# Performance work log

Measured on AMD Instinct MI355X. Metric: run time of the kernel, lower is better.

Reference implementation:

```python
import math
import jax, jax.numpy as jnp
import numpy as np

L = 3
EPS = 1e-06


def _geometry(H, W, L):
    """Replicates the Python-side region layout of the torch ramac() exactly."""
    ovr = 0.4
    steps = np.array([2, 3, 4, 5, 6, 7], dtype=np.float64)
    w = min(W, H)
    b = (max(H, W) - w) / (steps - 1)
    idx = int(np.argmin(np.abs((w ** 2 - w * b) / w ** 2 - ovr)))
    Wd = idx if H < W else 0
    Hd = idx if H > W else 0
    regions = []  # list of (i, j, wl) static ints
    for l in range(1, L + 1):
        wl = math.floor(2 * w / (l + 1))
        if wl == 0:
            continue
        wl2 = math.floor(wl / 2 - 1)
        bW = 0 if l + Wd == 1 else (W - wl) / (l + Wd - 1)
        cenW = [int(math.floor(wl2 + k * bW) - wl2) for k in range(l - 1 + Wd + 1)]
        bH = 0 if l + Hd == 1 else (H - wl) / (l + Hd - 1)
        cenH = [int(math.floor(wl2 + k * bH) - wl2) for k in range(l - 1 + Hd + 1)]
        for i in cenH:
            for j in cenW:
                regions.append((i, j, wl))
    return regions


def _weighted_mac(R, tt_region, eps):
    # R: [B, C, h, w]; tt_region: [B, h, w] bool
    vt = R.max(axis=(2, 3))  # [B, C] regional max-pool
    area = tt_region.shape[-2] * tt_region.shape[-1]
    # NOTE: faithful to torch: sum over batch too, divided only by region area
    wgt = tt_region.sum().astype(jnp.float32) / area
    wgt = jnp.where(wgt <= 1.0 / 3.0, jnp.zeros_like(wgt), wgt)
    nrm = jnp.linalg.norm(vt, axis=1, keepdims=True)  # L2 over channels
    return vt / (nrm + eps) * wgt


def _ramac(x, L, eps):
    B, C, H, W = x.shape
    s = x.sum(axis=1)                 # [B, H, W]
    tt = (s - s.mean()) > 0           # [B, H, W] attention mask (bool)
    v = _weighted_mac(x, tt, eps)     # global region
    for (i, j, wl) in _geometry(H, W, L):
        R = x[:, :, i:i + wl, j:j + wl]
        v = v + _weighted_mac(R, tt[:, i:i + wl, j:j + wl], eps)
    return v.reshape(B, C, 1, 1)


def setup_inputs() -> dict:
    key = jax.random.key(0)
    x = jax.random.normal(key, (16, 1024, 64, 64), dtype=jnp.float32)
    return {"x": x}


def reference(x):
    return _ramac(x, L, EPS)
```

## Files before the change

### kernel.cpp

```cpp
#include <hip/hip_runtime.h>
#include <math.h>


#define NB 16
#define NC 1024
#define G 16
#define NCHUNK (NC / G)

template <int ctrl, int rm, int bm>
__device__ __forceinline__ float maxdpp(float x) {
  int xi = __float_as_int(x);
  int yi = __builtin_amdgcn_update_dpp(xi, xi, ctrl, rm, bm, false);
  return fmaxf(x, __int_as_float(yi));
}
__device__ __forceinline__ float wave_max64(float x) {
  x = maxdpp<0x111, 0xf, 0xf>(x);
  x = maxdpp<0x112, 0xf, 0xf>(x);
  x = maxdpp<0x114, 0xf, 0xe>(x);
  x = maxdpp<0x118, 0xf, 0xc>(x);
  x = maxdpp<0x142, 0xa, 0xf>(x);
  x = maxdpp<0x143, 0x8, 0xf>(x);
  return x;
}
__device__ __forceinline__ float shflxor_max(float x, int m) {
  return fmaxf(x, __shfl_xor(x, m));
}

__global__ __launch_bounds__(256, 4) void k1_main(
    const float4* __restrict__ x, float4* __restrict__ vtp4,
    float4* __restrict__ spart4, float* __restrict__ total,
    int* __restrict__ cnt) {
  const int t = threadIdx.x;
  const int chunk = blockIdx.x;
  const int b = blockIdx.y;
  if (chunk == 0 && b == 0) {
    if (t == 0) *total = 0.f;
    if (t < 14) cnt[t] = 0;
  }
  const int fb = t & 15;
  const int r0t = t >> 4;
  const int w = t >> 6;
  const int L = t & 63;
  const float NEG = -INFINITY;
  const bool cAf = (fb <= 9), cAp = (fb == 10);
  const bool cBf = (fb >= 6), cBp = (fb == 5);
  const bool rAk2 = (r0t < 10);
  const bool rBk1 = (r0t >= 6);

  __shared__ float4 sm4[14][G];

  float4 sa0 = {0, 0, 0, 0}, sa1 = {0, 0, 0, 0}, sa2 = {0, 0, 0, 0},
         sa3 = {0, 0, 0, 0};
  const float4* img = x + (((size_t)(b * NC + chunk * G)) << 10);

  auto chain = [&](float V, float& outCE, float& outD) {
    float a = shflxor_max(V, 16);
    a = shflxor_max(a, 32);
    float b4 = maxdpp<0xB1, 0xf, 0xf>(a);
    b4 = maxdpp<0x4E, 0xf, 0xf>(b4);
    outD = fmaxf(b4, __shfl_xor(b4, 12));
    outCE = maxdpp<0x141, 0xf, 0xf>(b4);
  };

  auto process = [&](float4 v0, float4 v1, float4 v2, float4 v3, int ci) {
    sa0.x += v0.x; sa0.y += v0.y; sa0.z += v0.z; sa0.w += v0.w;
    sa1.x += v1.x; sa1.y += v1.y; sa1.z += v1.z; sa1.w += v1.w;
    sa2.x += v2.x; sa2.y += v2.y; sa2.z += v2.z; sa2.w += v2.w;
    sa3.x += v3.x; sa3.y += v3.y; sa3.z += v3.z; sa3.w += v3.w;

    float m0 = fmaxf(fmaxf(v0.x, v0.y), fmaxf(v0.z, v0.w));
    float m1 = fmaxf(fmaxf(v1.x, v1.y), fmaxf(v1.z, v1.w));
    float m2 = fmaxf(fmaxf(v2.x, v2.y), fmaxf(v2.z, v2.w));
    float m3 = fmaxf(fmaxf(v3.x, v3.y), fmaxf(v3.z, v3.w));
    float pA0 = fmaxf(v0.x, v0.y), pA1 = fmaxf(v1.x, v1.y);
    float pA2 = fmaxf(v2.x, v2.y), pA3 = fmaxf(v3.x, v3.y);
    float pB0 = fmaxf(v0.z, v0.w), pB1 = fmaxf(v1.z, v1.w);
    float pB2 = fmaxf(v2.z, v2.w), pB3 = fmaxf(v3.z, v3.w);

    float m01 = fmaxf(m0, m1), m12 = fmaxf(m1, m2), m23 = fmaxf(m2, m3);
    float MAm = fmaxf(m01, rAk2 ? m2 : NEG);
    float MBm = fmaxf(m23, rBk1 ? m1 : NEG);
    float MApA = fmaxf(fmaxf(pA0, pA1), rAk2 ? pA2 : NEG);
    float MApB = fmaxf(fmaxf(pB0, pB1), rAk2 ? pB2 : NEG);
    float MBpA = fmaxf(fmaxf(pA2, pA3), rBk1 ? pA1 : NEG);
    float MBpB = fmaxf(fmaxf(pB2, pB3), rBk1 ? pB1 : NEG);

    float g0 = fmaxf(m01, m23);
    float g1 = cAf ? MAm : (cAp ? MApA : NEG);
    float g2 = cBf ? MAm : (cBp ? MApB : NEG);
    float g3 = cAf ? MBm : (cAp ? MBpA : NEG);
    float g4 = cBf ? MBm : (cBp ? MBpB : NEG);
    g0 = wave_max64(g0); g1 = wave_max64(g1); g2 = wave_max64(g2);
    g3 = wave_max64(g3); g4 = wave_max64(g4);

    float ceC, dC, ceD, dD, ceE, dE;
    chain(m01, ceC, dC);
    chain(m12, ceD, dD);
    chain(m23, ceE, dE);

    float* smf = (float*)&sm4[0][0];
    const int o = (ci << 2) + w;
    const int RS = G * 4;
    if (L == 63) {
      smf[o]          = g0;  smf[o + 1 * RS] = g1;
      smf[o + 2 * RS] = g2;  smf[o + 3 * RS] = g3;
      smf[o + 4 * RS] = g4;
    }
    if (L == 0) {
      smf[o + 5 * RS] = ceC; smf[o + 8 * RS] = ceD; smf[o + 11 * RS] = ceE;
    }
    if (L == 4) {
      smf[o + 6 * RS] = dC;  smf[o + 9 * RS] = dD;  smf[o + 12 * RS] = dE;
    }
    if (L == 8) {
      smf[o + 7 * RS] = ceC; smf[o + 10 * RS] = ceD; smf[o + 13 * RS] = ceE;
    }
  };

  float4 v0 = img[t], v1 = img[t + 256], v2 = img[t + 512], v3 = img[t + 768];
  for (int ci = 0; ci < G - 1; ++ci) {
    const float4* q = img + (((size_t)(ci + 1)) << 10);
    float4 n0 = q[t], n1 = q[t + 256], n2 = q[t + 512], n3 = q[t + 768];
    process(v0, v1, v2, v3, ci);
    v0 = n0; v1 = n1; v2 = n2; v3 = n3;
  }
  process(v0, v1, v2, v3, G - 1);

  const int sb = ((chunk * NB + b) << 10);
  spart4[sb + t] = sa0;
  spart4[sb + t + 256] = sa1;
  spart4[sb + t + 512] = sa2;
  spart4[sb + t + 768] = sa3;

  __syncthreads();
  for (int i = t; i < 14 * G; i += 256) {
    const int r = i >> 4, ci = i & 15;
    vtp4[r * (NB * NC) + (b << 10) + chunk * G + ci] = sm4[r][ci];
  }
}

__global__ __launch_bounds__(256) void k2_mid(
    const float4* __restrict__ spart4, float4* __restrict__ s4,
    float* __restrict__ total, const float4* __restrict__ vtp4,
    float* __restrict__ vt, float* __restrict__ nrm) {
  const int blk = blockIdx.x;
  const int t = threadIdx.x;
  __shared__ float red[4];
  if (blk < 64) {
    const int id = blk * 256 + t;
    float4 acc = {0, 0, 0, 0};
    for (int ch = 0; ch < NCHUNK; ++ch) {
      float4 v = spart4[(ch << 14) + id];
      acc.x += v.x; acc.y += v.y; acc.z += v.z; acc.w += v.w;
    }
    s4[id] = acc;
    float ts = (acc.x + acc.y) + (acc.z + acc.w);
    for (int off = 1; off < 64; off <<= 1) ts += __shfl_xor(ts, off);
    if ((t & 63) == 0) atomicAdd(total, ts);
  } else {
    const int rb = blk - 64;
    float acc = 0.f;
#pragma unroll
    for (int k = 0; k < 4; ++k) {
      const int c = t + 256 * k;
      float4 v = vtp4[(rb << 10) + c];
      float m = fmaxf(fmaxf(v.x, v.y), fmaxf(v.z, v.w));
      vt[(rb << 10) + c] = m;
      acc += m * m;
    }
    for (int off = 1; off < 64; off <<= 1) acc += __shfl_xor(acc, off);
    if ((t & 63) == 0) red[t >> 6] = acc;
    __syncthreads();
    if (t == 0) nrm[rb] = sqrtf(red[0] + red[1] + red[2] + red[3]);
  }
}

__global__ __launch_bounds__(256) void k3_cnt(const float* __restrict__ s,
                                              const float* __restrict__ total,
                                              int* __restrict__ cnt) {
  const int b = blockIdx.x >> 2;
  const int q = blockIdx.x & 3;
  const int t = threadIdx.x;
  const float mean = *total * (1.0f / 65536.0f);
  int loc[14];
#pragma unroll
  for (int r = 0; r < 14; ++r) loc[r] = 0;
#pragma unroll
  for (int k = 0; k < 4; ++k) {
    const int p = t + 256 * (q * 4 + k);
    const int row = p >> 6, col = p & 63;
    const bool tt = s[(b << 12) + p] > mean;
    if (tt) {
      const bool rA = row < 42, rB = row >= 22, rC = row < 32;
      const bool rD = (row >= 16) && (row < 48), rE = row >= 32;
      const bool cA = col < 42, cB = col >= 22, cC = col < 32;
      const bool cD = (col >= 16) && (col < 48), cE = col >= 32;
      loc[0]++;
      loc[1] += rA && cA;  loc[2] += rA && cB;
      loc[3] += rB && cA;  loc[4] += rB && cB;
      loc[5] += rC && cC;  loc[6] += rC && cD;  loc[7] += rC && cE;
      loc[8] += rD && cC;  loc[9] += rD && cD;  loc[10] += rD && cE;
      loc[11] += rE && cC; loc[12] += rE && cD; loc[13] += rE && cE;
    }
  }
#pragma unroll
  for (int r = 0; r < 14; ++r) {
    int v = loc[r];
    for (int off = 1; off < 64; off <<= 1) v += __shfl_xor(v, off);
    if ((t & 63) == 0) atomicAdd(&cnt[r], v);
  }
}

__global__ __launch_bounds__(256) void k4_out(const float* __restrict__ vt,
                                              const float* __restrict__ nrm,
                                              const int* __restrict__ cnt,
                                              float* __restrict__ out) {
  const int id = blockIdx.x * 256 + threadIdx.x;
  const int b = id >> 10;
  float acc = 0.f;
#pragma unroll
  for (int r = 0; r < 14; ++r) {
    const float area = (r == 0) ? 4096.f : ((r <= 4) ? 1764.f : 1024.f);
    float wgt = (float)cnt[r] / area;
    if (wgt <= (1.0f / 3.0f)) wgt = 0.f;
    const float mult = (r == 0) ? 2.f : 1.f;
    acc += mult * wgt * vt[r * 16384 + id] / (nrm[r * 16 + b] + 1e-6f);
  }
  out[id] = acc;
}

extern "C" void kernel_launch(void* const* d_in, const int* in_sizes, int n_in,
                              void* d_out, int out_size, void* d_ws,
                              size_t ws_size, hipStream_t stream) {
  const float* x = (const float*)d_in[0];
  float* out = (float*)d_out;

  float* ws = (float*)d_ws;
  float* vtp = ws;
  float* spart = vtp + 917504;
  float* s = spart + 4194304;
  float* vt = s + 65536;
  float* nrm = vt + 229376;
  float* total = nrm + 224;
  int* cnt = (int*)(total + 1);

  k1_main<<<dim3(NCHUNK, NB), 256, 0, stream>>>(
      (const float4*)x, (float4*)vtp, (float4*)spart, total, cnt);
  k2_mid<<<64 + 224, 256, 0, stream>>>((const float4*)spart, (float4*)s, total,
                                       (const float4*)vtp, vt, nrm);
  k3_cnt<<<64, 256, 0, stream>>>(s, total, cnt);
  k4_out<<<64, 256, 0, stream>>>(vt, nrm, cnt, out);
}
```

Measured before the change: 413.0 us.

## Double channels per block and cut cross-lane reductions in regional max kernel

Each k1 block now handles 32 channels instead of 16. This halves the number of partial spatial-sum slabs written to and re-read from the workspace. The per-channel cross-lane max chain is rebuilt from DPP quad ops, a ds_swizzle and row mirror ops instead of several shfl_xor calls. The global-region max is now derived from the existing chain results rather than a separate full 64-lane reduction. The occupancy hint in launch_bounds is dropped, and the grid has fewer, longer-running blocks, which may reduce latency hiding.

```diff
diff --git a/kernel.cpp b/kernel.cpp
--- a/kernel.cpp
+++ b/kernel.cpp
@@ -4,7 +4,7 @@
 
 #define NB 16
 #define NC 1024
-#define G 16
+#define G 32
 #define NCHUNK (NC / G)
 
 template <int ctrl, int rm, int bm>
@@ -22,11 +22,15 @@
   x = maxdpp<0x143, 0x8, 0xf>(x);
   return x;
 }
+__device__ __forceinline__ float swz16_max(float x) {
+  int y = __builtin_amdgcn_ds_swizzle(__float_as_int(x), 0x401F);
+  return fmaxf(x, __int_as_float(y));
+}
 __device__ __forceinline__ float shflxor_max(float x, int m) {
   return fmaxf(x, __shfl_xor(x, m));
 }
 
-__global__ __launch_bounds__(256, 4) void k1_main(
+__global__ __launch_bounds__(256) void k1_main(
     const float4* __restrict__ x, float4* __restrict__ vtp4,
     float4* __restrict__ spart4, float* __restrict__ total,
     int* __restrict__ cnt) {
@@ -54,11 +58,11 @@
   const float4* img = x + (((size_t)(b * NC + chunk * G)) << 10);
 
   auto chain = [&](float V, float& outCE, float& outD) {
-    float a = shflxor_max(V, 16);
-    a = shflxor_max(a, 32);
-    float b4 = maxdpp<0xB1, 0xf, 0xf>(a);
+    float b4 = maxdpp<0xB1, 0xf, 0xf>(V);
     b4 = maxdpp<0x4E, 0xf, 0xf>(b4);
-    outD = fmaxf(b4, __shfl_xor(b4, 12));
+    b4 = swz16_max(b4);
+    b4 = shflxor_max(b4, 32);
+    outD = maxdpp<0x140, 0xf, 0xf>(b4);
     outCE = maxdpp<0x141, 0xf, 0xf>(b4);
   };
 
@@ -85,35 +89,37 @@
     float MBpA = fmaxf(fmaxf(pA2, pA3), rBk1 ? pA1 : NEG);
     float MBpB = fmaxf(fmaxf(pB2, pB3), rBk1 ? pB1 : NEG);
 
-    float g0 = fmaxf(m01, m23);
     float g1 = cAf ? MAm : (cAp ? MApA : NEG);
     float g2 = cBf ? MAm : (cBp ? MApB : NEG);
     float g3 = cAf ? MBm : (cAp ? MBpA : NEG);
     float g4 = cBf ? MBm : (cBp ? MBpB : NEG);
-    g0 = wave_max64(g0); g1 = wave_max64(g1); g2 = wave_max64(g2);
+    g1 = wave_max64(g1); g2 = wave_max64(g2);
     g3 = wave_max64(g3); g4 = wave_max64(g4);
 
-    float ceC, dC, ceD, dD, ceE, dE;
-    chain(m01, ceC, dC);
-    chain(m12, ceD, dD);
-    chain(m23, ceE, dE);
+    float ce01, d01, ce12, d12, ce23, d23;
+    chain(m01, ce01, d01);
+    chain(m12, ce12, d12);
+    chain(m23, ce23, d23);
+
+    float rf = fmaxf(ce01, ce23);
+    float r0v = maxdpp<0x140, 0xf, 0xf>(rf);
 
     float* smf = (float*)&sm4[0][0];
     const int o = (ci << 2) + w;
     const int RS = G * 4;
     if (L == 63) {
-      smf[o]          = g0;  smf[o + 1 * RS] = g1;
-      smf[o + 2 * RS] = g2;  smf[o + 3 * RS] = g3;
-      smf[o + 4 * RS] = g4;
+      smf[o + 1 * RS] = g1;  smf[o + 2 * RS] = g2;
+      smf[o + 3 * RS] = g3;  smf[o + 4 * RS] = g4;
     }
     if (L == 0) {
-      smf[o + 5 * RS] = ceC; smf[o + 8 * RS] = ceD; smf[o + 11 * RS] = ceE;
+      smf[o]          = r0v;
+      smf[o + 5 * RS] = ce01; smf[o + 8 * RS] = ce12; smf[o + 11 * RS] = ce23;
     }
     if (L == 4) {
-      smf[o + 6 * RS] = dC;  smf[o + 9 * RS] = dD;  smf[o + 12 * RS] = dE;
+      smf[o + 6 * RS] = d01;  smf[o + 9 * RS] = d12;  smf[o + 12 * RS] = d23;
     }
     if (L == 8) {
-      smf[o + 7 * RS] = ceC; smf[o + 10 * RS] = ceD; smf[o + 13 * RS] = ceE;
+      smf[o + 7 * RS] = ce01; smf[o + 10 * RS] = ce12; smf[o + 13 * RS] = ce23;
     }
   };
 
@@ -134,7 +140,7 @@
 
   __syncthreads();
   for (int i = t; i < 14 * G; i += 256) {
-    const int r = i >> 4, ci = i & 15;
+    const int r = i / G, ci = i % G;
     vtp4[r * (NB * NC) + (b << 10) + chunk * G + ci] = sm4[r][ci];
   }
 }
@@ -238,7 +244,7 @@
   float* ws = (float*)d_ws;
   float* vtp = ws;
   float* spart = vtp + 917504;
-  float* s = spart + 4194304;
+  float* s = spart + 2097152;
   float* vt = s + 65536;
   float* nrm = vt + 229376;
   float* total = nrm + 224;
```

Measured after the change: 411.4 us. No clear change (-0.4%).
